# Kernel optimization log

Hardware: AMD Instinct MI355X
Metric: run time of the kernel (lower is better)

## Reference

```python
import jax, jax.numpy as jnp
import numpy as np

B, S, E = 8, 4096, 768
NEG = jnp.float32(-1e30)


def setup_inputs() -> dict:
    key = jax.random.key(0)
    ks = jax.random.split(key, 9)
    full_ebd = jax.random.normal(ks[0], (B, S, E), dtype=jnp.float32)
    # first_idx in [64, S//2): end of question span (question tokens are 1..first_idx-1)
    first = jax.random.randint(ks[1], (B,), 64, S // 2)
    # second_idx in (first, S): end of context span (unused by the math but part of API)
    second = jax.random.randint(ks[2], (B,), S // 2 + 1, S)
    SEQ_idxes = jnp.stack([first, second], axis=1).astype(jnp.int64)
    w = 0.02
    Wq_w = jax.random.normal(ks[3], (E, E), dtype=jnp.float32) * w
    Wq_b = jax.random.normal(ks[4], (E,), dtype=jnp.float32) * w
    Wk_w = jax.random.normal(ks[5], (E, E), dtype=jnp.float32) * w
    Wk_b = jax.random.normal(ks[6], (E,), dtype=jnp.float32) * w
    Wv_w = jax.random.normal(ks[7], (E, E), dtype=jnp.float32) * w
    Wv_b = jax.random.normal(ks[8], (E,), dtype=jnp.float32) * w
    return {"full_ebd": full_ebd, "SEQ_idxes": SEQ_idxes,
            "Wq_w": Wq_w, "Wq_b": Wq_b, "Wk_w": Wk_w, "Wk_b": Wk_b,
            "Wv_w": Wv_w, "Wv_b": Wv_b}


def reference(full_ebd, SEQ_idxes, Wq_w, Wq_b, Wk_w, Wk_b, Wv_w, Wv_b):
    # Vectorized form of the ragged per-sample loop: queries attend to the
    # question tokens 1..first_idx-1 only; masking keys reproduces the slice.
    seq = full_ebd.shape[1]
    inv_sqrt_dk = jnp.float32(1.0 / np.sqrt(full_ebd.shape[-1]))
    Q = full_ebd @ Wq_w.T + Wq_b              # [B,S,E]
    K = full_ebd @ Wk_w.T + Wk_b              # [B,S,E]
    V = full_ebd @ Wv_w.T + Wv_b              # [B,S,E]
    first = SEQ_idxes[:, 0]                   # [B]
    j = jnp.arange(seq)
    key_mask = (j[None, :] >= 1) & (j[None, :] < first[:, None])  # [B,S]
    scores = jnp.einsum('bqe,bke->bqk', Q, K) * inv_sqrt_dk       # [B,S,S]
    scores = jnp.where(key_mask[:, None, :], scores, NEG)
    attn = jax.nn.softmax(scores, axis=-1)
    attn = attn * key_mask[:, None, :].astype(attn.dtype)  # exact zeros outside span
    H = jnp.einsum('bqk,bke->bqe', attn, V)   # [B,S,E]
    return H
```

## Files before the change

kernel.cpp:

```cpp
#include <hip/hip_runtime.h>
#include <hip/hip_bf16.h>
#include <cmath>

typedef __bf16 bf16x8 __attribute__((ext_vector_type(8)));
typedef __bf16 bf16x4 __attribute__((ext_vector_type(4)));
typedef float f32x4 __attribute__((ext_vector_type(4)));

#define GLOBAL_AS __attribute__((address_space(1)))
#define LDS_AS __attribute__((address_space(3)))

__device__ __forceinline__ void async_copy16(const void* g, void* l) {
    __builtin_amdgcn_global_load_lds((const GLOBAL_AS void*)g, (LDS_AS void*)l, 16, 0, 0);
}

__device__ inline int get_first(const int* __restrict__ seq, int b) {
    int stride = (seq[1] == 0) ? 4 : 2;
    return seq[b * stride];
}

__global__ __launch_bounds__(256) void cast_f32_bf16(const float* __restrict__ in,
                                                     __bf16* __restrict__ out, int n4) {
    int i = blockIdx.x * 256 + threadIdx.x;
    if (i >= n4) return;
    float4 v = ((const float4*)in)[i];
    bf16x4 o;
    o[0] = (__bf16)v.x; o[1] = (__bf16)v.y; o[2] = (__bf16)v.z; o[3] = (__bf16)v.w;
    ((bf16x4*)out)[i] = o;
}

__global__ __launch_bounds__(256) void cast3_f32_bf16(
    const float* __restrict__ a, const float* __restrict__ b, const float* __restrict__ c,
    __bf16* __restrict__ oa, __bf16* __restrict__ ob, __bf16* __restrict__ oc, int n4) {
    int i = blockIdx.x * 256 + threadIdx.x;
    if (i >= n4) return;
    const float* in = (blockIdx.y == 0) ? a : (blockIdx.y == 1) ? b : c;
    __bf16* out = (blockIdx.y == 0) ? oa : (blockIdx.y == 1) ? ob : oc;
    float4 v = ((const float4*)in)[i];
    bf16x4 o;
    o[0] = (__bf16)v.x; o[1] = (__bf16)v.y; o[2] = (__bf16)v.z; o[3] = (__bf16)v.w;
    ((bf16x4*)out)[i] = o;
}

__global__ __launch_bounds__(256) void zero_f32(float* __restrict__ p, int n4) {
    int i = blockIdx.x * 256 + threadIdx.x;
    if (i < n4) ((f32x4*)p)[i] = f32x4{0.f, 0.f, 0.f, 0.f};
}

template <int EPI>
__global__ __launch_bounds__(256, 4) void gemm_bt(
    const __bf16* __restrict__ A, int lda, long strideA,
    const __bf16* __restrict__ B, int ldb, long strideB,
    const float* __restrict__ bias,
    void* __restrict__ Cv, int ldc, long strideC,
    int Kfix, const int* __restrict__ seq, int exit_mode, int k_mode,
    float cs, float* __restrict__ rowsum) {
    int z = blockIdx.z;
    int m0 = blockIdx.x * 128, n0 = blockIdx.y * 128;
    int first = seq ? get_first(seq, z) : 0;
    if (exit_mode == 1 && m0 >= first) return;
    if (exit_mode == 2 && n0 >= first) return;
    int K = k_mode ? ((first + 63) & ~63) : Kfix;

    __shared__ char As[16384];
    __shared__ char Bs[16384];

    int tid = threadIdx.x;
    int lane = tid & 63, wid = tid >> 6;
    int waveM = (wid & 1) << 6, waveN = (wid >> 1) << 6;
    int quad = lane >> 4, l16 = lane & 15;

    int r0 = tid >> 3;
    int c8 = (tid & 7) ^ (r0 & 7);
    const __bf16* Ag = A + (long)z * strideA + (long)(m0 + r0) * lda + c8 * 8;
    const __bf16* Bg = B + (long)z * strideB + (long)(n0 + r0) * ldb + c8 * 8;

    f32x4 acc[4][4] = {};
    int xorv = (l16 & 7) << 4;

    for (int k0 = 0; k0 < K; k0 += 64) {
        __syncthreads();
#pragma unroll
        for (int r = 0; r < 4; ++r) {
            async_copy16(Ag + (long)(r * 32) * lda + k0, As + (tid + r * 256) * 16);
            async_copy16(Bg + (long)(r * 32) * ldb + k0, Bs + (tid + r * 256) * 16);
        }
        __syncthreads();
#pragma unroll
        for (int s = 0; s < 2; ++s) {
            int chunk = (((s << 2) + quad) << 4) ^ xorv;
            bf16x8 bfr[4];
#pragma unroll
            for (int j = 0; j < 4; ++j)
                bfr[j] = *(const bf16x8*)(Bs + (waveN + j * 16 + l16) * 128 + chunk);
#pragma unroll
            for (int i = 0; i < 4; ++i) {
                bf16x8 af = *(const bf16x8*)(As + (waveM + i * 16 + l16) * 128 + chunk);
#pragma unroll
                for (int j = 0; j < 4; ++j)
                    acc[i][j] = __builtin_amdgcn_mfma_f32_16x16x32_bf16(af, bfr[j], acc[i][j], 0, 0, 0);
            }
        }
    }

    if (EPI == 0) {
        __bf16* C = (__bf16*)Cv + (long)z * strideC;
#pragma unroll
        for (int i = 0; i < 4; ++i) {
            int rowb = m0 + waveM + i * 16 + quad * 4;
#pragma unroll
            for (int j = 0; j < 4; ++j) {
                int col = n0 + waveN + j * 16 + l16;
                float bv_ = bias[col];
#pragma unroll
                for (int r = 0; r < 4; ++r)
                    C[(long)(rowb + r) * ldc + col] = (__bf16)(acc[i][j][r] + bv_);
            }
        }
    } else if (EPI == 1) {
        __bf16* C = (__bf16*)Cv + (long)z * strideC;
#pragma unroll
        for (int i = 0; i < 4; ++i) {
            int rowb = m0 + waveM + i * 16 + quad * 4;
#pragma unroll
            for (int j = 0; j < 4; ++j) {
                int col = n0 + waveN + j * 16 + l16;
                float bv_ = bias[col];
                bf16x4 o;
#pragma unroll
                for (int r = 0; r < 4; ++r) o[r] = (__bf16)(acc[i][j][r] + bv_);
                *(bf16x4*)&C[(long)col * ldc + rowb] = o;
            }
        }
    } else if (EPI == 2) {
        __bf16* C = (__bf16*)Cv + (long)z * strideC;
        float* rs = rowsum + (long)z * 4096;
#pragma unroll
        for (int i = 0; i < 4; ++i) {
            int rowb = m0 + waveM + i * 16 + quad * 4;
            float sum[4] = {0.f, 0.f, 0.f, 0.f};
#pragma unroll
            for (int j = 0; j < 4; ++j) {
                int col = n0 + waveN + j * 16 + l16;
                bool valid = (col >= 1) && (col < first);
#pragma unroll
                for (int r = 0; r < 4; ++r) {
                    float e = valid ? exp2f(acc[i][j][r] * cs) : 0.0f;
                    __bf16 pb = (__bf16)e;
                    C[(long)(rowb + r) * ldc + col] = pb;
                    sum[r] += (float)pb;
                }
            }
#pragma unroll
            for (int r = 0; r < 4; ++r) {
                float v = sum[r];
                v += __shfl_xor(v, 8); v += __shfl_xor(v, 4);
                v += __shfl_xor(v, 2); v += __shfl_xor(v, 1);
                if (l16 == 0) atomicAdd(&rs[rowb + r], v);
            }
        }
    } else {
        float* C = (float*)Cv + (long)z * strideC;
        const float* rs = rowsum + (long)z * 4096;
#pragma unroll
        for (int i = 0; i < 4; ++i) {
            int rowb = m0 + waveM + i * 16 + quad * 4;
            float inv[4];
#pragma unroll
            for (int r = 0; r < 4; ++r) inv[r] = 1.0f / rs[rowb + r];
#pragma unroll
            for (int j = 0; j < 4; ++j) {
                int col = n0 + waveN + j * 16 + l16;
#pragma unroll
                for (int r = 0; r < 4; ++r)
                    C[(long)(rowb + r) * ldc + col] = acc[i][j][r] * inv[r];
            }
        }
    }
}

extern "C" void kernel_launch(void* const* d_in, const int* in_sizes, int n_in,
                              void* d_out, int out_size, void* d_ws, size_t ws_size,
                              hipStream_t stream) {
    const int B = 8, S = 4096, E = 768, SK = 2048;
    const float* ebd  = (const float*)d_in[0];
    const int*   seq  = (const int*)d_in[1];
    const float* Wq_w = (const float*)d_in[2];
    const float* Wq_b = (const float*)d_in[3];
    const float* Wk_w = (const float*)d_in[4];
    const float* Wk_b = (const float*)d_in[5];
    const float* Wv_w = (const float*)d_in[6];
    const float* Wv_b = (const float*)d_in[7];
    float* out = (float*)d_out;

    char* p = (char*)d_ws;
    __bf16* ebd_bf = (__bf16*)p; p += (size_t)B * S * E * 2;
    __bf16* wq = (__bf16*)p;     p += (size_t)E * E * 2;
    __bf16* wk = (__bf16*)p;     p += (size_t)E * E * 2;
    __bf16* wv = (__bf16*)p;     p += (size_t)E * E * 2;
    __bf16* Qb = (__bf16*)p;     p += (size_t)B * S * E * 2;
    __bf16* Kb = (__bf16*)p;     p += (size_t)B * SK * E * 2;
    __bf16* VT = (__bf16*)p;     p += (size_t)B * E * SK * 2;
    __bf16* Pb = (__bf16*)p;     p += (size_t)B * S * SK * 2;
    float* rowsum = (float*)p;   p += (size_t)B * S * 4;

    zero_f32<<<B * S / 4 / 256, 256, 0, stream>>>(rowsum, B * S / 4);
    cast_f32_bf16<<<(B * S * E / 4 + 255) / 256, 256, 0, stream>>>(ebd, ebd_bf, B * S * E / 4);
    cast3_f32_bf16<<<dim3((E * E / 4 + 255) / 256, 3), 256, 0, stream>>>(
        Wq_w, Wk_w, Wv_w, wq, wk, wv, E * E / 4);

    float cs = (1.0f / sqrtf((float)E)) * 1.44269504088896f;

    gemm_bt<0><<<dim3(B * S / 128, E / 128, 1), 256, 0, stream>>>(
        ebd_bf, E, 0, wq, E, 0, Wq_b, Qb, E, 0, E, nullptr, 0, 0, 0.f, nullptr);
    gemm_bt<0><<<dim3(SK / 128, E / 128, B), 256, 0, stream>>>(
        ebd_bf, E, (long)S * E, wk, E, 0, Wk_b, Kb, E, (long)SK * E, E, seq, 1, 0, 0.f, nullptr);
    gemm_bt<1><<<dim3(SK / 128, E / 128, B), 256, 0, stream>>>(
        ebd_bf, E, (long)S * E, wv, E, 0, Wv_b, VT, SK, (long)E * SK, E, seq, 1, 0, 0.f, nullptr);
    gemm_bt<2><<<dim3(S / 128, SK / 128, B), 256, 0, stream>>>(
        Qb, E, (long)S * E, Kb, E, (long)SK * E, nullptr, Pb, SK, (long)S * SK, E, seq, 2, 0, cs, rowsum);
    gemm_bt<3><<<dim3(S / 128, E / 128, B), 256, 0, stream>>>(
        Pb, SK, (long)S * SK, VT, SK, (long)E * SK, nullptr, out, E, (long)S * E, 0, seq, 0, 1, 0.f, rowsum);
}
```

Before: 410.3 us.

## Add 256x256-tile 8-wave GEMM with interleaved async loads for Q, QK, PV

Adds a new GEMM kernel with 256x256 output tiles and 512 threads. It uses double-buffered LDS fed by global_load_lds async copies, interleaved with MFMA phases, explicit s_barrier/waitcnt and s_setprio scheduling. The Q projection, the masked score GEMM and the PV GEMM now use this kernel, while K and V still use the old 128-tile kernel. The aim is more data reuse per tile and better overlap of loads with MFMA work, at the cost of higher register and LDS pressure (128KB LDS per block) and coarser tiles that waste more work on the ragged K range.

```diff
diff --git a/kernel.cpp b/kernel.cpp
--- a/kernel.cpp
+++ b/kernel.cpp
@@ -12,6 +12,11 @@
 __device__ __forceinline__ void async_copy16(const void* g, void* l) {
     __builtin_amdgcn_global_load_lds((const GLOBAL_AS void*)g, (LDS_AS void*)l, 16, 0, 0);
 }
+
+#define SBAR() asm volatile("s_barrier" ::: "memory")
+#define WAITLGKM0() asm volatile("s_waitcnt lgkmcnt(0)" ::: "memory")
+#define WAITVM4() asm volatile("s_waitcnt vmcnt(4)" ::: "memory")
+#define WAITVM0() asm volatile("s_waitcnt vmcnt(0)" ::: "memory")
 
 __device__ inline int get_first(const int* __restrict__ seq, int b) {
     int stride = (seq[1] == 0) ? 4 : 2;
@@ -116,7 +121,7 @@
                     C[(long)(rowb + r) * ldc + col] = (__bf16)(acc[i][j][r] + bv_);
             }
         }
-    } else if (EPI == 1) {
+    } else {
         __bf16* C = (__bf16*)Cv + (long)z * strideC;
 #pragma unroll
         for (int i = 0; i < 4; ++i) {
@@ -131,16 +136,206 @@
                 *(bf16x4*)&C[(long)col * ldc + rowb] = o;
             }
         }
+    }
+}
+
+template <int MI0, int NJ0>
+__device__ __forceinline__ void mq(f32x4 (&acc)[8][4], const bf16x8 (&av)[4][2],
+                                   const bf16x8 (&bv)[2][2]) {
+#pragma unroll
+    for (int i = 0; i < 4; ++i)
+#pragma unroll
+        for (int j = 0; j < 2; ++j)
+#pragma unroll
+            for (int ks = 0; ks < 2; ++ks)
+                acc[MI0 + i][NJ0 + j] = __builtin_amdgcn_mfma_f32_16x16x32_bf16(
+                    av[i][ks], bv[j][ks], acc[MI0 + i][NJ0 + j], 0, 0, 0);
+}
+
+template <int EPI>
+__global__ __launch_bounds__(512, 2) void gemm256(
+    const __bf16* __restrict__ A, int lda, long strideA,
+    const __bf16* __restrict__ B, int ldb, long strideB,
+    const float* __restrict__ bias,
+    void* __restrict__ Cv, int ldc, long strideC,
+    int Kfix, const int* __restrict__ seq, int exit_mode, int k_mode,
+    float cs, float* __restrict__ rowsum) {
+    int z = blockIdx.z;
+    int m0 = blockIdx.x * 256, n0 = blockIdx.y * 256;
+    int first = seq ? get_first(seq, z) : 0;
+    if (exit_mode == 2 && n0 >= first) return;
+    int K = k_mode ? ((first + 127) & ~127) : Kfix;
+    int np = K >> 7;
+
+    __shared__ char As[2][32768];
+    __shared__ char Bs[2][32768];
+
+    int tid = threadIdx.x;
+    int lane = tid & 63, wid = tid >> 6;
+    int wrb = (wid >> 2) << 7;
+    int wcb = (wid & 3) << 6;
+    int quad = lane >> 4, l16 = lane & 15;
+    int xr = l16 & 7;
+
+    int rg = tid >> 3;
+    int src_c8 = (tid & 7) ^ (rg & 7);
+    const __bf16* Ag = A + (long)z * strideA + (long)(m0 + rg) * lda + src_c8 * 8;
+    const __bf16* Bg = B + (long)z * strideB + (long)(n0 + rg) * ldb + src_c8 * 8;
+
+#define STA(bb, h, kk) do { \
+    async_copy16(Ag + (long)((h) * 128) * lda + (kk),      &As[bb][(h) * 16384 + tid * 16]); \
+    async_copy16(Ag + (long)((h) * 128 + 64) * lda + (kk), &As[bb][(h) * 16384 + 8192 + tid * 16]); } while (0)
+#define STB(bb, h, kk) do { \
+    async_copy16(Bg + (long)((h) * 128) * ldb + (kk),      &Bs[bb][(h) * 16384 + tid * 16]); \
+    async_copy16(Bg + (long)((h) * 128 + 64) * ldb + (kk), &Bs[bb][(h) * 16384 + 8192 + tid * 16]); } while (0)
+#define RA(bb, row, ks) (*(const bf16x8*)(&As[bb][(row) * 128 + ((((ks) * 4 + quad) ^ xr) << 4)]))
+#define RB(bb, row, ks) (*(const bf16x8*)(&Bs[bb][(row) * 128 + ((((ks) * 4 + quad) ^ xr) << 4)]))
+
+    f32x4 acc[8][4] = {};
+    bf16x8 av[4][2], b0[2][2], b1[2][2];
+
+    STB(0, 0, 0); STA(0, 0, 0); STA(0, 1, 0); STB(0, 1, 0);
+    STB(1, 0, 64); STA(1, 0, 64);
+    WAITVM4();
+    SBAR();
+
+    for (int it = 0; it < np; ++it) {
+        int k0 = it << 7;
+        bool s2 = (it + 1) < np;
+
+#pragma unroll
+        for (int i = 0; i < 4; ++i) {
+            av[i][0] = RA(0, wrb + i * 16 + l16, 0);
+            av[i][1] = RA(0, wrb + i * 16 + l16, 1);
+        }
+#pragma unroll
+        for (int j = 0; j < 2; ++j) {
+            b0[j][0] = RB(0, wcb + j * 16 + l16, 0);
+            b0[j][1] = RB(0, wcb + j * 16 + l16, 1);
+        }
+        STA(1, 1, k0 + 64);
+        SBAR(); WAITLGKM0();
+        __builtin_amdgcn_s_setprio(1);
+        mq<0, 0>(acc, av, b0);
+        __builtin_amdgcn_s_setprio(0);
+        SBAR();
+
+#pragma unroll
+        for (int j = 0; j < 2; ++j) {
+            b1[j][0] = RB(0, wcb + 32 + j * 16 + l16, 0);
+            b1[j][1] = RB(0, wcb + 32 + j * 16 + l16, 1);
+        }
+        STB(1, 1, k0 + 64);
+        SBAR(); WAITLGKM0();
+        __builtin_amdgcn_s_setprio(1);
+        mq<0, 2>(acc, av, b1);
+        __builtin_amdgcn_s_setprio(0);
+        SBAR();
+
+#pragma unroll
+        for (int i = 0; i < 4; ++i) {
+            av[i][0] = RA(0, wrb + 64 + i * 16 + l16, 0);
+            av[i][1] = RA(0, wrb + 64 + i * 16 + l16, 1);
+        }
+        if (s2) STB(0, 0, k0 + 128);
+        SBAR(); WAITLGKM0();
+        __builtin_amdgcn_s_setprio(1);
+        mq<4, 0>(acc, av, b0);
+        __builtin_amdgcn_s_setprio(0);
+        SBAR();
+
+        if (s2) {
+            STA(0, 0, k0 + 128);
+            WAITVM4();
+        } else {
+            WAITVM0();
+        }
+        SBAR();
+        __builtin_amdgcn_s_setprio(1);
+        mq<4, 2>(acc, av, b1);
+        __builtin_amdgcn_s_setprio(0);
+        SBAR();
+
+#pragma unroll
+        for (int i = 0; i < 4; ++i) {
+            av[i][0] = RA(1, wrb + i * 16 + l16, 0);
+            av[i][1] = RA(1, wrb + i * 16 + l16, 1);
+        }
+#pragma unroll
+        for (int j = 0; j < 2; ++j) {
+            b0[j][0] = RB(1, wcb + j * 16 + l16, 0);
+            b0[j][1] = RB(1, wcb + j * 16 + l16, 1);
+        }
+        if (s2) STA(0, 1, k0 + 128);
+        SBAR(); WAITLGKM0();
+        __builtin_amdgcn_s_setprio(1);
+        mq<0, 0>(acc, av, b0);
+        __builtin_amdgcn_s_setprio(0);
+        SBAR();
+
+#pragma unroll
+        for (int j = 0; j < 2; ++j) {
+            b1[j][0] = RB(1, wcb + 32 + j * 16 + l16, 0);
+            b1[j][1] = RB(1, wcb + 32 + j * 16 + l16, 1);
+        }
+        if (s2) STB(0, 1, k0 + 128);
+        SBAR(); WAITLGKM0();
+        __builtin_amdgcn_s_setprio(1);
+        mq<0, 2>(acc, av, b1);
+        __builtin_amdgcn_s_setprio(0);
+        SBAR();
+
+#pragma unroll
+        for (int i = 0; i < 4; ++i) {
+            av[i][0] = RA(1, wrb + 64 + i * 16 + l16, 0);
+            av[i][1] = RA(1, wrb + 64 + i * 16 + l16, 1);
+        }
+        if (s2) STB(1, 0, k0 + 192);
+        SBAR(); WAITLGKM0();
+        __builtin_amdgcn_s_setprio(1);
+        mq<4, 0>(acc, av, b0);
+        __builtin_amdgcn_s_setprio(0);
+        SBAR();
+
+        if (s2) {
+            STA(1, 0, k0 + 192);
+            WAITVM4();
+        }
+        SBAR();
+        __builtin_amdgcn_s_setprio(1);
+        mq<4, 2>(acc, av, b1);
+        __builtin_amdgcn_s_setprio(0);
+        SBAR();
+    }
+#undef STA
+#undef STB
+#undef RA
+#undef RB
+
+    if (EPI == 0) {
+        __bf16* C = (__bf16*)Cv + (long)z * strideC;
+#pragma unroll
+        for (int i = 0; i < 8; ++i) {
+            int rowb = m0 + wrb + i * 16 + quad * 4;
+#pragma unroll
+            for (int j = 0; j < 4; ++j) {
+                int col = n0 + wcb + j * 16 + l16;
+                float bv_ = bias[col];
+#pragma unroll
+                for (int r = 0; r < 4; ++r)
+                    C[(long)(rowb + r) * ldc + col] = (__bf16)(acc[i][j][r] + bv_);
+            }
+        }
     } else if (EPI == 2) {
         __bf16* C = (__bf16*)Cv + (long)z * strideC;
         float* rs = rowsum + (long)z * 4096;
 #pragma unroll
-        for (int i = 0; i < 4; ++i) {
-            int rowb = m0 + waveM + i * 16 + quad * 4;
+        for (int i = 0; i < 8; ++i) {
+            int rowb = m0 + wrb + i * 16 + quad * 4;
             float sum[4] = {0.f, 0.f, 0.f, 0.f};
 #pragma unroll
             for (int j = 0; j < 4; ++j) {
-                int col = n0 + waveN + j * 16 + l16;
+                int col = n0 + wcb + j * 16 + l16;
                 bool valid = (col >= 1) && (col < first);
 #pragma unroll
                 for (int r = 0; r < 4; ++r) {
@@ -162,14 +357,14 @@
         float* C = (float*)Cv + (long)z * strideC;
         const float* rs = rowsum + (long)z * 4096;
 #pragma unroll
-        for (int i = 0; i < 4; ++i) {
-            int rowb = m0 + waveM + i * 16 + quad * 4;
+        for (int i = 0; i < 8; ++i) {
+            int rowb = m0 + wrb + i * 16 + quad * 4;
             float inv[4];
 #pragma unroll
             for (int r = 0; r < 4; ++r) inv[r] = 1.0f / rs[rowb + r];
 #pragma unroll
             for (int j = 0; j < 4; ++j) {
-                int col = n0 + waveN + j * 16 + l16;
+                int col = n0 + wcb + j * 16 + l16;
 #pragma unroll
                 for (int r = 0; r < 4; ++r)
                     C[(long)(rowb + r) * ldc + col] = acc[i][j][r] * inv[r];
@@ -210,14 +405,14 @@
 
     float cs = (1.0f / sqrtf((float)E)) * 1.44269504088896f;
 
-    gemm_bt<0><<<dim3(B * S / 128, E / 128, 1), 256, 0, stream>>>(
+    gemm256<0><<<dim3(B * S / 256, E / 256, 1), 512, 0, stream>>>(
         ebd_bf, E, 0, wq, E, 0, Wq_b, Qb, E, 0, E, nullptr, 0, 0, 0.f, nullptr);
     gemm_bt<0><<<dim3(SK / 128, E / 128, B), 256, 0, stream>>>(
         ebd_bf, E, (long)S * E, wk, E, 0, Wk_b, Kb, E, (long)SK * E, E, seq, 1, 0, 0.f, nullptr);
     gemm_bt<1><<<dim3(SK / 128, E / 128, B), 256, 0, stream>>>(
         ebd_bf, E, (long)S * E, wv, E, 0, Wv_b, VT, SK, (long)E * SK, E, seq, 1, 0, 0.f, nullptr);
-    gemm_bt<2><<<dim3(S / 128, SK / 128, B), 256, 0, stream>>>(
+    gemm256<2><<<dim3(S / 256, SK / 256, B), 512, 0, stream>>>(
         Qb, E, (long)S * E, Kb, E, (long)SK * E, nullptr, Pb, SK, (long)S * SK, E, seq, 2, 0, cs, rowsum);
-    gemm_bt<3><<<dim3(S / 128, E / 128, B), 256, 0, stream>>>(
+    gemm256<3><<<dim3(S / 256, E / 256, B), 512, 0, stream>>>(
         Pb, SK, (long)S * SK, VT, SK, (long)E * SK, nullptr, out, E, (long)S * E, 0, seq, 0, 1, 0.f, rowsum);
 }
```

After: 455.2 us. 1.11x slower.
